# Kernel tuning notes

Hardware: AMD Instinct MI355X
Metric: run time of the kernel (lower is better)

Reference implementation:

```python
import jax, jax.numpy as jnp
import numpy as np
import math

B, C, H, W, D = 4, 64, 16, 16, 16
TEMB = 256
GROUPS = 16
EPS = 1e-5


def group_norm(x, gamma, beta, groups=GROUPS, eps=EPS):
    # x: [B, C, H, W, D]
    b, c, h, w, d = x.shape
    xg = x.reshape(b, groups, c // groups, h, w, d)
    mu = jnp.mean(xg, axis=(2, 3, 4, 5), keepdims=True)
    var = jnp.var(xg, axis=(2, 3, 4, 5), keepdims=True)
    xn = ((xg - mu) / jnp.sqrt(var + eps)).reshape(b, c, h, w, d)
    return xn * gamma[None, :, None, None, None] + beta[None, :, None, None, None]


def swish(x):
    return x * jax.nn.sigmoid(x)


def conv3d(x, w, b=None):
    y = jax.lax.conv_general_dilated(
        x, w, window_strides=(1, 1, 1), padding='SAME',
        dimension_numbers=('NCDHW', 'OIDHW', 'NCDHW'))
    if b is not None:
        y = y + b[None, :, None, None, None]
    return y


def setup_inputs() -> dict:
    key = jax.random.key(0)
    ks = jax.random.split(key, 16)
    s = lambda fan: 1.0 / math.sqrt(fan)
    inp = {
        'x': jax.random.normal(ks[0], (B, C, H, W, D), jnp.float32),
        'time_emb': jax.random.normal(ks[1], (B, TEMB), jnp.float32),
        # block1: GroupNorm + Conv3d(C->C, 3)
        'gn1_g': jnp.ones((C,), jnp.float32),
        'gn1_b': jnp.zeros((C,), jnp.float32),
        'conv1_w': jax.random.normal(ks[2], (C, C, 3, 3, 3), jnp.float32) * s(C * 27),
        'conv1_b': jnp.zeros((C,), jnp.float32),
        # time-embedding MLP: Linear(TEMB -> C)
        'mlp_w': jax.random.normal(ks[3], (C, TEMB), jnp.float32) * s(TEMB),
        'mlp_b': jnp.zeros((C,), jnp.float32),
        # block2: GroupNorm + Conv3d(C->C, 3)
        'gn2_g': jnp.ones((C,), jnp.float32),
        'gn2_b': jnp.zeros((C,), jnp.float32),
        'conv2_w': jax.random.normal(ks[4], (C, C, 3, 3, 3), jnp.float32) * s(C * 27),
        'conv2_b': jnp.zeros((C,), jnp.float32),
        # attention: GroupNorm, qkv 1x1 conv (no bias), out 1x1 conv
        'agn_g': jnp.ones((C,), jnp.float32),
        'agn_b': jnp.zeros((C,), jnp.float32),
        'qkv_w': jax.random.normal(ks[5], (3 * C, C), jnp.float32) * s(C),
        'out_w': jax.random.normal(ks[6], (C, C), jnp.float32) * s(C),
        'out_b': jnp.zeros((C,), jnp.float32),
    }
    return inp


def reference(x, time_emb, gn1_g, gn1_b, conv1_w, conv1_b, mlp_w, mlp_b,
              gn2_g, gn2_b, conv2_w, conv2_b, agn_g, agn_b, qkv_w, out_w, out_b):
    # --- ResnetBlock ---
    h = conv3d(swish(group_norm(x, gn1_g, gn1_b)), conv1_w, conv1_b)
    t = swish(time_emb) @ mlp_w.T + mlp_b                    # [B, C]
    h = h + t[:, :, None, None, None]
    h = conv3d(swish(group_norm(h, gn2_g, gn2_b)), conv2_w, conv2_b)
    x = h + x                                                # res_conv is Identity (dim == dim_out)
    # --- SelfAttention (n_head = 1) ---
    b, c, hh, ww, dd = x.shape
    n = hh * ww * dd
    norm = group_norm(x, agn_g, agn_b)
    qkv = jnp.einsum('oc,bchwd->bohwd', qkv_w, norm).reshape(b, 3 * c, n)
    q, k, v = jnp.split(qkv, 3, axis=1)                      # [B, C, N] each
    attn = jnp.einsum('bcn,bcm->bnm', q, k) / math.sqrt(c)   # [B, N, N]
    attn = jax.nn.softmax(attn, axis=-1)
    o = jnp.einsum('bnm,bcm->bcn', attn, v).reshape(b, c, hh, ww, dd)
    o = jnp.einsum('oc,bchwd->bohwd', out_w, o) + out_b[None, :, None, None, None]
    return o + x
```

## Files before the change

kernel.cpp:

```cpp
#include <hip/hip_runtime.h>
#include <math.h>

#define B 4
#define C 64
#define G 16
#define CPG 4
#define N 4096
#define TEMB 256

using f16x8 = __attribute__((ext_vector_type(8))) _Float16;
using f16x4 = __attribute__((ext_vector_type(4))) _Float16;
using f32x4 = __attribute__((ext_vector_type(4))) float;
using f32x16 = __attribute__((ext_vector_type(16))) float;
using h2 = __attribute__((ext_vector_type(2))) __fp16;

#define QSCALE 0.18033688f
#define SHIFT2 4.328085f

__device__ __forceinline__ int swzi(int row, int ci) {
  return (((ci >> 3) ^ (row & 7)) << 3) | (ci & 7);
}

__device__ __forceinline__ void gn_fin(const float2* pstats, const float* gamma,
                                       const float* beta, int b, int c,
                                       float& sc, float& sh) {
  int g = c >> 2;
  const float2* ps = pstats + ((size_t)(b * 16 + g)) * 4;
  float2 p0 = ps[0], p1 = ps[1], p2 = ps[2], p3 = ps[3];
  const float inv = 1.f / 16384.f;
  float mean = (p0.x + p1.x + p2.x + p3.x) * inv;
  float msq = (p0.y + p1.y + p2.y + p3.y) * inv;
  float var = msq - mean * mean;
  float rstd = rsqrtf(var + 1e-5f);
  sc = gamma[c] * rstd;
  sh = beta[c] - mean * sc;
}

__global__ void __launch_bounds__(256) k_gnpart(const float* __restrict__ x,
                                                float2* __restrict__ pstats) {
  int bx = blockIdx.x;
  const float4* xp = (const float4*)(x + (size_t)bx * 4096);
  float s = 0.f, s2 = 0.f;
#pragma unroll
  for (int kk = 0; kk < 4; kk++) {
    float4 v = xp[threadIdx.x + kk * 256];
    s += v.x + v.y + v.z + v.w;
    s2 += v.x * v.x + v.y * v.y + v.z * v.z + v.w * v.w;
  }
#pragma unroll
  for (int off = 32; off > 0; off >>= 1) {
    s += __shfl_down(s, off);
    s2 += __shfl_down(s2, off);
  }
  __shared__ float ls[4], ls2[4];
  int lane = threadIdx.x & 63, wid = threadIdx.x >> 6;
  if (lane == 0) { ls[wid] = s; ls2[wid] = s2; }
  __syncthreads();
  if (threadIdx.x == 0) {
    float2 r;
    r.x = ls[0] + ls[1] + ls[2] + ls[3];
    r.y = ls2[0] + ls2[1] + ls2[2] + ls2[3];
    pstats[bx] = r;
  }
}

__global__ void __launch_bounds__(256) k_prepgn(const float* __restrict__ w1,
                                                const float* __restrict__ w2,
                                                const float* __restrict__ temb,
                                                const float* __restrict__ mlp_w,
                                                const float* __restrict__ mlp_b,
                                                const float* __restrict__ x,
                                                _Float16* __restrict__ wf1,
                                                _Float16* __restrict__ wf2,
                                                float* __restrict__ tb,
                                                float2* __restrict__ pstats) {
  int bx = blockIdx.x, tid = threadIdx.x;
  __shared__ float sw[TEMB];
  __shared__ float part[4][64];
  __shared__ float ls[4], ls2[4];
  if (bx < 54) {
    const float* w = (bx < 27) ? w1 : w2;
    _Float16* wf = (bx < 27) ? wf1 : wf2;
    int tap = (bx < 27) ? bx : bx - 27;
    int co = tid >> 2, ci0 = (tid & 3) * 16;
    union { _Float16 hh[16]; f16x8 v[2]; } pk;
#pragma unroll
    for (int r = 0; r < 16; r++)
      pk.hh[r] = (_Float16)w[((size_t)(co * 64 + ci0 + r)) * 27 + tap];
    f16x8* dst = (f16x8*)(wf + ((size_t)tap * 64 + co) * 64 + ci0);
    dst[0] = pk.v[0]; dst[1] = pk.v[1];
  } else if (bx < 58) {
    int b = bx - 54;
    {
      float v = temb[b * TEMB + tid];
      sw[tid] = v / (1.f + __expf(-v));
    }
    __syncthreads();
    int co = tid & 63, seg = tid >> 6;
    float acc = 0.f;
#pragma unroll 16
    for (int k = 0; k < 64; k++) acc += sw[seg * 64 + k] * mlp_w[co * TEMB + seg * 64 + k];
    part[seg][co] = acc;
    __syncthreads();
    if (tid < 64) tb[b * C + tid] = part[0][tid] + part[1][tid] + part[2][tid] + part[3][tid] + mlp_b[tid];
  } else {
    int bx2 = bx - 58;
    const float4* xp = (const float4*)(x + (size_t)bx2 * 4096);
    float s = 0.f, s2 = 0.f;
#pragma unroll
    for (int kk = 0; kk < 4; kk++) {
      float4 v = xp[tid + kk * 256];
      s += v.x + v.y + v.z + v.w;
      s2 += v.x * v.x + v.y * v.y + v.z * v.z + v.w * v.w;
    }
#pragma unroll
    for (int off = 32; off > 0; off >>= 1) {
      s += __shfl_down(s, off);
      s2 += __shfl_down(s2, off);
    }
    int lane = tid & 63, wid = tid >> 6;
    if (lane == 0) { ls[wid] = s; ls2[wid] = s2; }
    __syncthreads();
    if (tid == 0) {
      float2 r;
      r.x = ls[0] + ls[1] + ls[2] + ls[3];
      r.y = ls2[0] + ls2[1] + ls2[2] + ls2[3];
      pstats[bx2] = r;
    }
  }
}

__global__ void __launch_bounds__(256) k_conv3f(const float* __restrict__ in,
                                                const float2* __restrict__ pstats,
                                                const float* __restrict__ gamma,
                                                const float* __restrict__ beta,
                                                const _Float16* __restrict__ wf,
                                                const float* __restrict__ bias,
                                                const float* __restrict__ addvec,
                                                const float* __restrict__ residual,
                                                float* __restrict__ out) {
  int bx = blockIdx.x;
  int b = bx >> 6, h = (bx >> 2) & 15, nog = bx & 3;
  int tid = threadIdx.x;
  int wv = tid >> 6, lane = tid & 63, hi = lane >> 5, l31 = lane & 31;
  int cw = wv >> 1, nw = wv & 1;
  __shared__ _Float16 a3[3][96][64];
  __shared__ _Float16 wl[2][64][64];
  __shared__ float2 scsh[64];
  if (tid < 64) {
    float sc, sh;
    gn_fin(pstats, gamma, beta, b, tid, sc, sh);
    float2 r; r.x = sc; r.y = sh;
    scsh[tid] = r;
  }
  __syncthreads();
  int w0 = nog * 4 - 1;
  for (int i = tid; i < 2304; i += 256) {
    int r = i / 768, rem = i % 768;
    int ci8 = rem / 96, ns = rem % 96;
    int wp = w0 + (ns >> 4), dd = ns & 15;
    int hin = h + r - 1;
    f16x8 val = {};
    if ((unsigned)hin < 16u && (unsigned)wp < 16u) {
      const float* src = in + (((size_t)(b * 64 + ci8 * 8) * 16 + hin) * 256) + wp * 16 + dd;
      union { _Float16 hh[8]; f16x8 v; } pk;
#pragma unroll
      for (int j = 0; j < 8; j++) {
        float v = src[(size_t)j * 4096];
        float2 ss = scsh[ci8 * 8 + j];
        float t = v * ss.x + ss.y;
        pk.hh[j] = (_Float16)(t / (1.f + __expf(-t)));
      }
      val = pk.v;
    }
    *(f16x8*)&a3[r][ns][swzi(ns, ci8 * 8)] = val;
  }
#pragma unroll
  for (int q = 0; q < 2; q++) {
    int chunk = tid + q * 256;
    int co = chunk >> 3, ci8 = chunk & 7;
    f16x8 v = *(const f16x8*)(wf + (size_t)co * 64 + ci8 * 8);
    *(f16x8*)&wl[0][co][swzi(co, ci8 * 8)] = v;
  }
  f32x16 acc = {};
  __syncthreads();
  int cur = 0;
  int co_r = cw * 32 + l31;
  int n_loc = nw * 32 + l31;
  int wrow = n_loc >> 4;
  int d = n_loc & 15;
  for (int t = 0; t < 27; t++) {
    f16x8 pw0 = {}, pw1 = {};
    if (t < 26) {
      pw0 = *(const f16x8*)(wf + ((size_t)(t + 1) * 64 + (tid >> 3)) * 64 + (tid & 7) * 8);
      pw1 = *(const f16x8*)(wf + ((size_t)(t + 1) * 64 + ((tid + 256) >> 3)) * 64 + (tid & 7) * 8);
    }
    int kw = (t / 3) % 3, kd = t % 3, kh = t / 9;
    int wpl = wrow + kw;
    int dp = d + kd - 1;
    bool ok = (unsigned)dp < 16u;
    int ns = wpl * 16 + dp;
#pragma unroll
    for (int c4 = 0; c4 < 4; c4++) {
      int ci = c4 * 16 + hi * 8;
      f16x8 af = *(const f16x8*)&wl[cur][co_r][swzi(co_r, ci)];
      f16x8 bf = {};
      if (ok) bf = *(const f16x8*)&a3[kh][ns][swzi(ns, ci)];
      acc = __builtin_amdgcn_mfma_f32_32x32x16_f16(af, bf, acc, 0, 0, 0);
    }
    if (t < 26) {
      *(f16x8*)&wl[cur ^ 1][tid >> 3][swzi(tid >> 3, (tid & 7) * 8)] = pw0;
      *(f16x8*)&wl[cur ^ 1][(tid + 256) >> 3][swzi((tid + 256) >> 3, (tid & 7) * 8)] = pw1;
      __syncthreads();
      cur ^= 1;
    }
  }
  int nq = nog * 64 + n_loc;
#pragma unroll
  for (int r = 0; r < 16; r++) {
    int co = cw * 32 + (r & 3) + 8 * (r >> 2) + 4 * hi;
    size_t off = (((size_t)(b * 64 + co)) * 16 + h) * 256 + nq;
    float vv = acc[r] + bias[co] + (addvec ? addvec[b * 64 + co] : 0.f);
    if (residual) vv += residual[off];
    out[off] = vv;
  }
}

__global__ void __launch_bounds__(256) k_qkv(const float* __restrict__ x2,
                                             const float2* __restrict__ pstats,
                                             const float* __restrict__ gamma,
                                             const float* __restrict__ beta,
                                             const float* __restrict__ w,
                                             _Float16* __restrict__ qh, _Float16* __restrict__ kh,
                                             _Float16* __restrict__ vh) {
  int b = blockIdx.x >> 6, nt = blockIdx.x & 63;
  int n0 = nt * 64;
  __shared__ __align__(16) float xl[64][64];
  __shared__ float wl[192 * 64];
  int tid = threadIdx.x;
  for (int i = tid; i < 192 * 64; i += 256) wl[i] = w[i];
  {
    int c = tid >> 2, seg = tid & 3;
    float sc, sh;
    gn_fin(pstats, gamma, beta, b, c, sc, sh);
    const float4* src = (const float4*)(x2 + ((size_t)(b * C + c)) * N + n0);
    float4* dst = (float4*)&xl[c][seg * 16];
#pragma unroll
    for (int j = 0; j < 4; j++) {
      float4 v = src[seg * 4 + j];
      v.x = v.x * sc + sh; v.y = v.y * sc + sh; v.z = v.z * sc + sh; v.w = v.w * sc + sh;
      dst[j] = v;
    }
  }
  __syncthreads();
  int nq = tid & 15, og = tid >> 4;
  float4 acc[12];
#pragma unroll
  for (int j = 0; j < 12; j++) acc[j] = make_float4(0.f, 0.f, 0.f, 0.f);
  for (int c = 0; c < 64; c++) {
    float4 xv = *(const float4*)&xl[c][nq * 4];
#pragma unroll
    for (int j = 0; j < 12; j++) {
      float wv = wl[(og * 12 + j) * 64 + c];
      acc[j].x += wv * xv.x; acc[j].y += wv * xv.y; acc[j].z += wv * xv.z; acc[j].w += wv * xv.w;
    }
  }
#pragma unroll
  for (int j = 0; j < 12; j++) {
    int o3 = og * 12 + j;
    if (o3 >= 128) {
      f16x4 pv;
      pv[0] = (_Float16)acc[j].x; pv[1] = (_Float16)acc[j].y;
      pv[2] = (_Float16)acc[j].z; pv[3] = (_Float16)acc[j].w;
      int c = o3 - 128;
      int t = (n0 >> 4) + (nq >> 2);
      *(f16x4*)(vh + ((size_t)(b * 256 + t) * 64 + c) * 16 + (nq & 3) * 4) = pv;
    }
  }
  __syncthreads();
#pragma unroll
  for (int j = 0; j < 12; j++) {
    int o3 = og * 12 + j;
    if (o3 < 64) {
      float4 v = acc[j];
      v.x *= QSCALE; v.y *= QSCALE; v.z *= QSCALE; v.w *= QSCALE;
      *(float4*)&xl[o3][nq * 4] = v;
    }
  }
  __syncthreads();
  {
    int n_ = tid >> 2, cs = (tid & 3) * 16;
    union { _Float16 hh[16]; uint4 u[2]; } pk;
#pragma unroll
    for (int r = 0; r < 16; r++) pk.hh[r] = (_Float16)xl[cs + r][n_];
    uint4* dst = (uint4*)(qh + ((size_t)b * N + n0 + n_) * 64 + cs);
    dst[0] = pk.u[0]; dst[1] = pk.u[1];
  }
  __syncthreads();
#pragma unroll
  for (int j = 0; j < 12; j++) {
    int o3 = og * 12 + j;
    if (o3 >= 64 && o3 < 128) *(float4*)&xl[o3 - 64][nq * 4] = acc[j];
  }
  __syncthreads();
  {
    int n_ = tid >> 2, cs = (tid & 3) * 16;
    union { _Float16 hh[16]; uint4 u[2]; } pk;
#pragma unroll
    for (int r = 0; r < 16; r++) pk.hh[r] = (_Float16)xl[cs + r][n_];
    uint4* dst = (uint4*)(kh + ((size_t)b * N + n0 + n_) * 64 + cs);
    dst[0] = pk.u[0]; dst[1] = pk.u[1];
  }
}

__global__ void __launch_bounds__(256) k_attn(const _Float16* __restrict__ q,
                                              const _Float16* __restrict__ k,
                                              const _Float16* __restrict__ v,
                                              _Float16* __restrict__ po,
                                              float* __restrict__ pl) {
  int bx = blockIdx.x;
  int s = bx >> 8, b = (bx >> 6) & 3, nt = bx & 63;
  int n0 = nt * 64;
  int tid = threadIdx.x;
  int wv = tid >> 6, lane = tid & 63, lg = lane >> 4, ll = lane & 15;
  __shared__ float ol[64][72];
  __shared__ float lsum[4][64];
  const _Float16* qp = q + (size_t)b * N * 64;
  f16x8 qf[4][2];
#pragma unroll
  for (int qb = 0; qb < 4; qb++)
#pragma unroll
    for (int ch = 0; ch < 2; ch++)
      qf[qb][ch] = *(const f16x8*)(qp + (size_t)(n0 + qb * 16 + ll) * 64 + ch * 32 + lg * 8);
  f32x4 oacc[4][4] = {};
  f32x4 lfrag[4] = {};
  const f16x4 ones = {(_Float16)1.f, (_Float16)1.f, (_Float16)1.f, (_Float16)1.f};
  const _Float16* kptr = k + (size_t)b * N * 64 + (size_t)(s * 1024 + wv * 16 + ll) * 64 + lg * 8;
  const _Float16* vptr = v + ((size_t)(b * 256 + s * 64 + wv) * 64 + ll) * 16 + lg * 4;
  f16x8 kf0 = *(const f16x8*)(kptr);
  f16x8 kf1 = *(const f16x8*)(kptr + 32);
  f16x4 vf[4];
#pragma unroll
  for (int cb = 0; cb < 4; cb++) vf[cb] = *(const f16x4*)(vptr + cb * 256);
  for (int it = 0; it < 16; it++) {
    const _Float16* kptrn = kptr + 4096;
    const _Float16* vptrn = vptr + 4096;
    f32x4 sv[4];
    __builtin_amdgcn_s_setprio(1);
#pragma unroll
    for (int qb = 0; qb < 4; qb++) {
      f32x4 z = {-SHIFT2, -SHIFT2, -SHIFT2, -SHIFT2};
      z = __builtin_amdgcn_mfma_f32_16x16x32_f16(kf0, qf[qb][0], z, 0, 0, 0);
      sv[qb] = __builtin_amdgcn_mfma_f32_16x16x32_f16(kf1, qf[qb][1], z, 0, 0, 0);
    }
    __builtin_amdgcn_s_setprio(0);
    f16x8 nk0 = *(const f16x8*)(kptrn);
    f16x8 nk1 = *(const f16x8*)(kptrn + 32);
    f16x4 nv[4];
#pragma unroll
    for (int cb = 0; cb < 4; cb++) nv[cb] = *(const f16x4*)(vptrn + cb * 256);
    f16x4 pk[4];
#pragma unroll
    for (int qb = 0; qb < 4; qb++) {
      float e0 = __builtin_amdgcn_exp2f(sv[qb][0]);
      float e1 = __builtin_amdgcn_exp2f(sv[qb][1]);
      float e2 = __builtin_amdgcn_exp2f(sv[qb][2]);
      float e3 = __builtin_amdgcn_exp2f(sv[qb][3]);
      union { h2 h[2]; f16x4 v4; } u;
      u.h[0] = __builtin_amdgcn_cvt_pkrtz(e0, e1);
      u.h[1] = __builtin_amdgcn_cvt_pkrtz(e2, e3);
      pk[qb] = u.v4;
    }
    __builtin_amdgcn_s_setprio(1);
#pragma unroll
    for (int qb = 0; qb < 4; qb++) {
#pragma unroll
      for (int cb = 0; cb < 4; cb++)
        oacc[qb][cb] = __builtin_amdgcn_mfma_f32_16x16x16f16(vf[cb], pk[qb], oacc[qb][cb], 0, 0, 0);
      lfrag[qb] = __builtin_amdgcn_mfma_f32_16x16x16f16(ones, pk[qb], lfrag[qb], 0, 0, 0);
    }
    __builtin_amdgcn_s_setprio(0);
    kf0 = nk0; kf1 = nk1;
#pragma unroll
    for (int cb = 0; cb < 4; cb++) vf[cb] = nv[cb];
    kptr = kptrn; vptr = vptrn;
  }
  if (lane < 16) {
#pragma unroll
    for (int qb = 0; qb < 4; qb++) lsum[wv][qb * 16 + lane] = lfrag[qb][0];
  }
  for (int w = 0; w < 4; w++) {
    __syncthreads();
    if (wv == w) {
#pragma unroll
      for (int qb = 0; qb < 4; qb++)
#pragma unroll
        for (int cb = 0; cb < 4; cb++) {
          float* a = &ol[qb * 16 + ll][cb * 16 + 4 * lg];
          if (w == 0) {
            *(f32x4*)a = oacc[qb][cb];
          } else {
            f32x4 t = *(f32x4*)a;
            t += oacc[qb][cb];
            *(f32x4*)a = t;
          }
        }
    }
  }
  __syncthreads();
  {
    int n = tid >> 2, cq = (tid & 3) * 16;
    float lt = lsum[0][n] + lsum[1][n] + lsum[2][n] + lsum[3][n];
    float inv = 1.f / lt;
    union { _Float16 hh[16]; uint4 u[2]; } pk2;
#pragma unroll
    for (int j = 0; j < 16; j++) pk2.hh[j] = (_Float16)(ol[n][cq + j] * inv);
    uint4* dst = (uint4*)(po + ((size_t)(s * 4 + b) * N + n0 + n) * 64 + cq);
    dst[0] = pk2.u[0]; dst[1] = pk2.u[1];
    if (tid < 64)
      pl[(size_t)(s * 4 + b) * N + n0 + tid] =
          lsum[0][tid] + lsum[1][tid] + lsum[2][tid] + lsum[3][tid];
  }
}

__global__ void __launch_bounds__(256) k_outproj(const _Float16* __restrict__ po,
                                                 const float* __restrict__ pl,
                                                 const float* __restrict__ w,
                                                 const float* __restrict__ bias,
                                                 const float* __restrict__ x2,
                                                 float* __restrict__ out) {
  int b = blockIdx.x >> 6, nt = blockIdx.x & 63;
  int n0 = nt * 64;
  __shared__ __align__(16) float wl2[64][68];
  __shared__ __align__(16) float ol[64][68];
  __shared__ float wsc[4][64];
  int tid = threadIdx.x;
  if (tid < 64) {
    float l0 = pl[((size_t)(0 * 4 + b)) * N + n0 + tid];
    float l1 = pl[((size_t)(1 * 4 + b)) * N + n0 + tid];
    float l2 = pl[((size_t)(2 * 4 + b)) * N + n0 + tid];
    float l3 = pl[((size_t)(3 * 4 + b)) * N + n0 + tid];
    float inv = 1.f / (l0 + l1 + l2 + l3);
    wsc[0][tid] = l0 * inv; wsc[1][tid] = l1 * inv;
    wsc[2][tid] = l2 * inv; wsc[3][tid] = l3 * inv;
  }
  for (int i = tid; i < 4096; i += 256) wl2[i >> 6][i & 63] = w[i];
  __syncthreads();
  for (int base = tid; base < 1024; base += 256) {
    int n = base >> 4, c0 = (base & 15) * 4;
    float a0 = 0.f, a1 = 0.f, a2 = 0.f, a3 = 0.f;
#pragma unroll
    for (int s = 0; s < 4; s++) {
      f16x4 pv = *(const f16x4*)&po[((size_t)(s * 4 + b) * N + n0 + n) * 64 + c0];
      float wsv = wsc[s][n];
      a0 += (float)pv[0] * wsv; a1 += (float)pv[1] * wsv;
      a2 += (float)pv[2] * wsv; a3 += (float)pv[3] * wsv;
    }
    ol[n][c0] = a0; ol[n][c0 + 1] = a1; ol[n][c0 + 2] = a2; ol[n][c0 + 3] = a3;
  }
  __syncthreads();
  int co = tid & 63, ng = tid >> 6;
  float acc16[16];
#pragma unroll
  for (int i = 0; i < 16; i++) acc16[i] = 0.f;
  for (int c4 = 0; c4 < 16; c4++) {
    float4 wv = *(const float4*)&wl2[co][c4 * 4];
#pragma unroll
    for (int i = 0; i < 16; i++) {
      float4 ov = *(const float4*)&ol[ng * 16 + i][c4 * 4];
      acc16[i] += wv.x * ov.x + wv.y * ov.y + wv.z * ov.z + wv.w * ov.w;
    }
  }
  float bv = bias[co];
  __syncthreads();
#pragma unroll
  for (int i = 0; i < 16; i++) ol[ng * 16 + i][co] = acc16[i] + bv;
  __syncthreads();
  for (int kk = 0; kk < 16; kk++) {
    int i = tid + kk * 256;
    int c2 = i >> 6, nl = i & 63;
    size_t idx = ((size_t)(b * C + c2)) * N + n0 + nl;
    out[idx] = ol[nl][c2] + x2[idx];
  }
}

extern "C" void kernel_launch(void* const* d_in, const int* in_sizes, int n_in,
                              void* d_out, int out_size, void* d_ws, size_t ws_size,
                              hipStream_t stream) {
  (void)in_sizes; (void)n_in; (void)out_size; (void)ws_size;
  const float* x       = (const float*)d_in[0];
  const float* temb    = (const float*)d_in[1];
  const float* gn1_g   = (const float*)d_in[2];
  const float* gn1_b   = (const float*)d_in[3];
  const float* conv1_w = (const float*)d_in[4];
  const float* conv1_b = (const float*)d_in[5];
  const float* mlp_w   = (const float*)d_in[6];
  const float* mlp_b   = (const float*)d_in[7];
  const float* gn2_g   = (const float*)d_in[8];
  const float* gn2_b   = (const float*)d_in[9];
  const float* conv2_w = (const float*)d_in[10];
  const float* conv2_b = (const float*)d_in[11];
  const float* agn_g   = (const float*)d_in[12];
  const float* agn_b   = (const float*)d_in[13];
  const float* qkv_w   = (const float*)d_in[14];
  const float* out_w   = (const float*)d_in[15];
  const float* out_b   = (const float*)d_in[16];
  float* out = (float*)d_out;
  float* ws = (float*)d_ws;
  const size_t F = 1048576;
  float* h        = ws;
  float* x2       = ws + F;
  _Float16* qh    = (_Float16*)(ws + 2 * F);
  _Float16* khb   = qh + F;
  _Float16* vhb   = khb + F;
  float2* pst1 = (float2*)(vhb + F);
  float2* pst2 = pst1 + 256;
  float2* pst3 = pst2 + 256;
  float* tb    = (float*)(pst3 + 256);
  _Float16* wf1 = (_Float16*)(tb + 256);
  _Float16* wf2 = wf1 + 27 * 64 * 64;
  _Float16* po  = wf2 + 27 * 64 * 64;
  float* pl     = (float*)(po + 4 * F);

  k_prepgn<<<314, 256, 0, stream>>>(conv1_w, conv2_w, temb, mlp_w, mlp_b, x,
                                    wf1, wf2, tb, pst1);
  k_conv3f<<<256, 256, 0, stream>>>(x, pst1, gn1_g, gn1_b, wf1, conv1_b, tb, nullptr, h);
  k_gnpart<<<256, 256, 0, stream>>>(h, pst2);
  k_conv3f<<<256, 256, 0, stream>>>(h, pst2, gn2_g, gn2_b, wf2, conv2_b, nullptr, x, x2);
  k_gnpart<<<256, 256, 0, stream>>>(x2, pst3);
  k_qkv<<<256, 256, 0, stream>>>(x2, pst3, agn_g, agn_b, qkv_w, qh, khb, vhb);
  k_attn<<<1024, 256, 0, stream>>>(qh, khb, vhb, po, pl);
  k_outproj<<<256, 256, 0, stream>>>(po, pl, out_w, out_b, x2, out);
}
```

Measured before the change: 114.5 us.

## Fuse GroupNorm statistics into conv epilogue and remap attention blocks per XCD

```diff
diff --git a/kernel.cpp b/kernel.cpp
--- a/kernel.cpp
+++ b/kernel.cpp
@@ -36,32 +36,30 @@
   sh = beta[c] - mean * sc;
 }
 
-__global__ void __launch_bounds__(256) k_gnpart(const float* __restrict__ x,
-                                                float2* __restrict__ pstats) {
-  int bx = blockIdx.x;
-  const float4* xp = (const float4*)(x + (size_t)bx * 4096);
-  float s = 0.f, s2 = 0.f;
-#pragma unroll
-  for (int kk = 0; kk < 4; kk++) {
-    float4 v = xp[threadIdx.x + kk * 256];
-    s += v.x + v.y + v.z + v.w;
-    s2 += v.x * v.x + v.y * v.y + v.z * v.z + v.w * v.w;
-  }
-#pragma unroll
-  for (int off = 32; off > 0; off >>= 1) {
-    s += __shfl_down(s, off);
-    s2 += __shfl_down(s2, off);
-  }
-  __shared__ float ls[4], ls2[4];
-  int lane = threadIdx.x & 63, wid = threadIdx.x >> 6;
-  if (lane == 0) { ls[wid] = s; ls2[wid] = s2; }
-  __syncthreads();
-  if (threadIdx.x == 0) {
-    float2 r;
-    r.x = ls[0] + ls[1] + ls[2] + ls[3];
-    r.y = ls2[0] + ls2[1] + ls2[2] + ls2[3];
-    pstats[bx] = r;
-  }
+__device__ __forceinline__ void gn_fin2(const float2* red, const float* gamma,
+                                        const float* beta, int b, int c,
+                                        float& sc, float& sh) {
+  float2 r = red[b * 16 + (c >> 2)];
+  const float inv = 1.f / 16384.f;
+  float mean = r.x * inv;
+  float var = r.y * inv - mean * mean;
+  float rstd = rsqrtf(var + 1e-5f);
+  sc = gamma[c] * rstd;
+  sh = beta[c] - mean * sc;
+}
+
+__global__ void k_gnred(const float2* __restrict__ blkstats, float2* __restrict__ red) {
+  int tid = threadIdx.x;
+  int pair = tid >> 2, q = tid & 3;
+  int b = pair >> 4, g = pair & 15;
+  float sx = 0.f, sy = 0.f;
+  for (int i = 0; i < 16; i++) {
+    float2 v = blkstats[(size_t)(b * 64 + q * 16 + i) * 16 + g];
+    sx += v.x; sy += v.y;
+  }
+  sx += __shfl_xor(sx, 1); sy += __shfl_xor(sy, 1);
+  sx += __shfl_xor(sx, 2); sy += __shfl_xor(sy, 2);
+  if (q == 0) { float2 r; r.x = sx; r.y = sy; red[pair] = r; }
 }
 
 __global__ void __launch_bounds__(256) k_prepgn(const float* __restrict__ w1,
@@ -138,7 +136,9 @@
                                                 const float* __restrict__ bias,
                                                 const float* __restrict__ addvec,
                                                 const float* __restrict__ residual,
-                                                float* __restrict__ out) {
+                                                float* __restrict__ out,
+                                                float2* __restrict__ blkstats,
+                                                int mode) {
   int bx = blockIdx.x;
   int b = bx >> 6, h = (bx >> 2) & 15, nog = bx & 3;
   int tid = threadIdx.x;
@@ -147,12 +147,15 @@
   __shared__ _Float16 a3[3][96][64];
   __shared__ _Float16 wl[2][64][64];
   __shared__ float2 scsh[64];
+  __shared__ float2 sg[16];
   if (tid < 64) {
     float sc, sh;
-    gn_fin(pstats, gamma, beta, b, tid, sc, sh);
+    if (mode == 0) gn_fin(pstats, gamma, beta, b, tid, sc, sh);
+    else gn_fin2(pstats, gamma, beta, b, tid, sc, sh);
     float2 r; r.x = sc; r.y = sh;
     scsh[tid] = r;
   }
+  if (tid >= 64 && tid < 80) { sg[tid - 64].x = 0.f; sg[tid - 64].y = 0.f; }
   __syncthreads();
   int w0 = nog * 4 - 1;
   for (int i = tid; i < 2304; i += 256) {
@@ -216,6 +219,7 @@
     }
   }
   int nq = nog * 64 + n_loc;
+  float gs[4] = {0.f, 0.f, 0.f, 0.f}, gs2[4] = {0.f, 0.f, 0.f, 0.f};
 #pragma unroll
   for (int r = 0; r < 16; r++) {
     int co = cw * 32 + (r & 3) + 8 * (r >> 2) + 4 * hi;
@@ -223,11 +227,30 @@
     float vv = acc[r] + bias[co] + (addvec ? addvec[b * 64 + co] : 0.f);
     if (residual) vv += residual[off];
     out[off] = vv;
-  }
+    gs[r >> 2] += vv;
+    gs2[r >> 2] += vv * vv;
+  }
+#pragma unroll
+  for (int off2 = 1; off2 < 32; off2 <<= 1)
+#pragma unroll
+    for (int rq = 0; rq < 4; rq++) {
+      gs[rq] += __shfl_xor(gs[rq], off2);
+      gs2[rq] += __shfl_xor(gs2[rq], off2);
+    }
+  if (l31 == 0) {
+#pragma unroll
+    for (int rq = 0; rq < 4; rq++) {
+      int g = cw * 8 + 2 * rq + hi;
+      atomicAdd(&sg[g].x, gs[rq]);
+      atomicAdd(&sg[g].y, gs2[rq]);
+    }
+  }
+  __syncthreads();
+  if (tid < 16) blkstats[(size_t)bx * 16 + tid] = sg[tid];
 }
 
 __global__ void __launch_bounds__(256) k_qkv(const float* __restrict__ x2,
-                                             const float2* __restrict__ pstats,
+                                             const float2* __restrict__ red,
                                              const float* __restrict__ gamma,
                                              const float* __restrict__ beta,
                                              const float* __restrict__ w,
@@ -242,7 +265,7 @@
   {
     int c = tid >> 2, seg = tid & 3;
     float sc, sh;
-    gn_fin(pstats, gamma, beta, b, c, sc, sh);
+    gn_fin2(red, gamma, beta, b, c, sc, sh);
     const float4* src = (const float4*)(x2 + ((size_t)(b * C + c)) * N + n0);
     float4* dst = (float4*)&xl[c][seg * 16];
 #pragma unroll
@@ -319,7 +342,10 @@
                                               _Float16* __restrict__ po,
                                               float* __restrict__ pl) {
   int bx = blockIdx.x;
-  int s = bx >> 8, b = (bx >> 6) & 3, nt = bx & 63;
+  int xcd = bx & 7, i6 = bx >> 3;
+  int nt = i6 & 63, phi = i6 >> 6;
+  int p = phi * 8 + xcd;
+  int s = p >> 2, b = p & 3;
   int n0 = nt * 64;
   int tid = threadIdx.x;
   int wv = tid >> 6, lane = tid & 63, lg = lane >> 4, ll = lane & 15;
@@ -514,21 +540,25 @@
   _Float16* khb   = qh + F;
   _Float16* vhb   = khb + F;
   float2* pst1 = (float2*)(vhb + F);
-  float2* pst2 = pst1 + 256;
-  float2* pst3 = pst2 + 256;
-  float* tb    = (float*)(pst3 + 256);
+  float* tb    = (float*)(pst1 + 256);
   _Float16* wf1 = (_Float16*)(tb + 256);
   _Float16* wf2 = wf1 + 27 * 64 * 64;
   _Float16* po  = wf2 + 27 * 64 * 64;
   float* pl     = (float*)(po + 4 * F);
+  float2* pstb1 = (float2*)(pl + 65536);
+  float2* pstb2 = pstb1 + 4096;
+  float2* red2  = pstb2 + 4096;
+  float2* red3  = red2 + 64;
 
   k_prepgn<<<314, 256, 0, stream>>>(conv1_w, conv2_w, temb, mlp_w, mlp_b, x,
                                     wf1, wf2, tb, pst1);
-  k_conv3f<<<256, 256, 0, stream>>>(x, pst1, gn1_g, gn1_b, wf1, conv1_b, tb, nullptr, h);
-  k_gnpart<<<256, 256, 0, stream>>>(h, pst2);
-  k_conv3f<<<256, 256, 0, stream>>>(h, pst2, gn2_g, gn2_b, wf2, conv2_b, nullptr, x, x2);
-  k_gnpart<<<256, 256, 0, stream>>>(x2, pst3);
-  k_qkv<<<256, 256, 0, stream>>>(x2, pst3, agn_g, agn_b, qkv_w, qh, khb, vhb);
+  k_conv3f<<<256, 256, 0, stream>>>(x, pst1, gn1_g, gn1_b, wf1, conv1_b, tb, nullptr,
+                                    h, pstb1, 0);
+  k_gnred<<<1, 256, 0, stream>>>(pstb1, red2);
+  k_conv3f<<<256, 256, 0, stream>>>(h, (const float2*)red2, gn2_g, gn2_b, wf2, conv2_b,
+                                    nullptr, x, x2, pstb2, 1);
+  k_gnred<<<1, 256, 0, stream>>>(pstb2, red3);
+  k_qkv<<<256, 256, 0, stream>>>(x2, (const float2*)red3, agn_g, agn_b, qkv_w, qh, khb, vhb);
   k_attn<<<1024, 256, 0, stream>>>(qh, khb, vhb, po, pl);
   k_outproj<<<256, 256, 0, stream>>>(po, pl, out_w, out_b, x2, out);
 }
```

New measurement: 119.1 us. 4.1% more time.
